# Kernel tuning notes

Hardware: AMD Instinct MI355X
Metric: run time of the kernel (lower is better)

The kernel has to match this reference:

```python
import jax, jax.numpy as jnp
import numpy as np

B, L, P, C, K, NL, DF = 32, 512, 96, 512, 8, 2, 512
CK = C // K
EPS = 1e-5


def setup_inputs() -> dict:
    key = jax.random.key(0)
    ks = jax.random.split(key, 6)
    s = lambda k, shape, fan: jax.random.normal(k, shape, jnp.float32) / np.float32(np.sqrt(fan))
    return dict(
        x=jax.random.normal(ks[0], (B, L, C), jnp.float32),
        cluster_ids=jnp.arange(C, dtype=jnp.int32),
        rev_w=jnp.ones((C,), jnp.float32),
        rev_b=jnp.zeros((C,), jnp.float32),
        Wt=s(ks[1], (K, NL, L, L), L),
        bt=jnp.zeros((K, NL, L), jnp.float32),
        ln1_g=jnp.ones((K, NL, CK), jnp.float32),
        ln1_b=jnp.zeros((K, NL, CK), jnp.float32),
        Wf1=s(ks[2], (K, NL, CK, DF), CK),
        bf1=jnp.zeros((K, NL, DF), jnp.float32),
        Wf2=s(ks[3], (K, NL, DF, CK), DF),
        bf2=jnp.zeros((K, NL, CK), jnp.float32),
        ln2_g=jnp.ones((K, NL, CK), jnp.float32),
        ln2_b=jnp.zeros((K, NL, CK), jnp.float32),
        Wout=s(ks[4], (K, L, P), L),
        bout=jnp.zeros((K, P), jnp.float32),
    )


def _ln(y, g, b):
    # y: [K,B,L,Ck]; g,b: [K,Ck] -- per-cluster layernorm over channel dim
    m = y.mean(-1, keepdims=True)
    v = y.var(-1, keepdims=True)
    return (y - m) * jax.lax.rsqrt(v + EPS) * g[:, None, None, :] + b[:, None, None, :]


def reference(x, cluster_ids, rev_w, rev_b, Wt, bt, ln1_g, ln1_b,
              Wf1, bf1, Wf2, bf2, ln2_g, ln2_b, Wout, bout):
    # RevIN norm (instance norm over time axis)
    mean = x.mean(axis=1, keepdims=True)
    std = jnp.sqrt(x.var(axis=1, keepdims=True) + EPS)
    xn = (x - mean) / std * rev_w + rev_b

    Kc = Wt.shape[0]
    Ck = cluster_ids.shape[0] // Kc
    assign = cluster_ids % Kc                 # hard cluster assignment per channel
    perm = jnp.argsort(assign)                # stable -> groups channels by cluster
    idx = perm.reshape(Kc, Ck)                # [K, Ck] channel ids per cluster

    # gather: [B,L,K,Ck] -> [K,B,L,Ck]
    xg = jnp.transpose(xn[:, :, idx], (2, 0, 1, 3))

    for l in range(Wt.shape[1]):
        # time mixing: Linear over seq dim, per cluster
        y = _ln(xg, ln1_g[:, l], ln1_b[:, l])
        y = jax.nn.relu(jnp.einsum('kblc,klm->kbmc', y, Wt[:, l]) + bt[:, l][:, None, :, None])
        xg = xg + y
        # feature mixing: Linear over channel dim, per cluster
        y = _ln(xg, ln2_g[:, l], ln2_b[:, l])
        y = jax.nn.relu(jnp.einsum('kblc,kcf->kblf', y, Wf1[:, l]) + bf1[:, l][:, None, None, :])
        y = jnp.einsum('kblf,kfc->kblc', y, Wf2[:, l]) + bf2[:, l][:, None, None, :]
        xg = xg + y

    # temporal projection seq_len -> pred_len: [K,B,P,Ck]
    out = jnp.einsum('kblc,klp->kbpc', xg, Wout) + bout[:, None, :, None]

    # scatter back to full channel layout
    flat = jnp.transpose(out, (1, 2, 0, 3)).reshape(x.shape[0], Wout.shape[-1], -1)
    full = jnp.zeros_like(flat).at[:, :, perm].set(flat)

    # RevIN denorm
    return (full - rev_b) / rev_w * std + mean
```

## Files before the change

kernel.cpp:

```cpp
#include <hip/hip_runtime.h>

typedef unsigned short u16;
typedef unsigned int   u32;
typedef __attribute__((ext_vector_type(8))) __bf16 bf16x8;
typedef __attribute__((ext_vector_type(4))) float  f32x4;

#define DEV __device__ __forceinline__

namespace {

constexpr int B_  = 32;
constexpr int L_  = 512;
constexpr int P_  = 96;
constexpr int C_  = 512;
constexpr int K_  = 8;
constexpr int NL_ = 2;
constexpr int DF_ = 512;
constexpr int CK_ = 64;
constexpr float EPS_ = 1e-5f;

DEV float bf2f(u16 u){ union { u32 i; float f; } t; t.i = ((u32)u) << 16; return t.f; }
DEV u16 f2bf(float f){ union { float f; u32 i; } t; t.f = f;
  u32 r = t.i + 0x7fffu + ((t.i >> 16) & 1u); return (u16)(r >> 16); }
DEV u16 f2bfn(float f){ __bf16 h = (__bf16)f; u16 u; __builtin_memcpy(&u, &h, 2); return u; }
DEV float LD(const void* p, size_t i, int bf){
  return bf ? bf2f(((const u16*)p)[i]) : ((const float*)p)[i];
}

__global__ __launch_bounds__(256) void k_probe(const u32* __restrict__ x, int* __restrict__ flag){
  int cnt = 0;
  for (int i = threadIdx.x; i < 4096; i += 256){
    u32 w = x[i];
    u32 e = (w >> 7) & 0xFFu;
    cnt += (e >= 0x70u && e <= 0x8Fu) ? 1 : 0;
  }
#pragma unroll
  for (int o = 32; o > 0; o >>= 1) cnt += __shfl_xor(cnt, o);
  __shared__ int s[4];
  if ((threadIdx.x & 63) == 0) s[threadIdx.x >> 6] = cnt;
  __syncthreads();
  if (threadIdx.x == 0) flag[0] = (s[0] + s[1] + s[2] + s[3] > 2048) ? 1 : 0;
}

__global__ __launch_bounds__(512) void k_sort(const int* __restrict__ cid, int* __restrict__ idx){
  __shared__ int bkt[C_];
  __shared__ int cnt[K_];
  __shared__ int off[K_];
  int c = threadIdx.x;
  int v = cid[c] % K_; if (v < 0) v += K_;
  bkt[c] = v;
  __syncthreads();
  if (c < K_){ int n = 0; for (int i = 0; i < C_; i++) n += (bkt[i] == c); cnt[c] = n; }
  __syncthreads();
  if (c == 0){ int s = 0; for (int k = 0; k < K_; k++){ off[k] = s; s += cnt[k]; } }
  __syncthreads();
  int r = 0;
  for (int i = 0; i < c; i++) r += (bkt[i] == bkt[c]);
  idx[off[bkt[c]] + r] = c;
}

__global__ __launch_bounds__(256) void k_trans(const void* __restrict__ in, u16* __restrict__ out,
                                               int R, int Cn, const int* __restrict__ flagp){
  __shared__ u16 t[32][36];
  int bf = *flagp;
  int z = blockIdx.z;
  int r0 = blockIdx.y * 32, c0 = blockIdx.x * 32;
  size_t base = (size_t)z * R * Cn;
  int tid = threadIdx.x;
  int i = tid >> 3, j4 = (tid & 7) * 4;
  size_t off = base + (size_t)(r0 + i) * Cn + c0 + j4;
  if (bf){
    ushort4 v = *reinterpret_cast<const ushort4*>((const u16*)in + off);
    t[i][j4 + 0] = v.x; t[i][j4 + 1] = v.y; t[i][j4 + 2] = v.z; t[i][j4 + 3] = v.w;
  } else {
    float4 v = *reinterpret_cast<const float4*>((const float*)in + off);
    t[i][j4 + 0] = f2bf(v.x); t[i][j4 + 1] = f2bf(v.y); t[i][j4 + 2] = f2bf(v.z); t[i][j4 + 3] = f2bf(v.w);
  }
  __syncthreads();
  ushort4 w;
  w.x = t[j4 + 0][i]; w.y = t[j4 + 1][i]; w.z = t[j4 + 2][i]; w.w = t[j4 + 3][i];
  *reinterpret_cast<ushort4*>(out + base + (size_t)(c0 + i) * R + r0 + j4) = w;
}

__global__ __launch_bounds__(512) void k_stats1(const void* __restrict__ x,
                                                float* __restrict__ psum, float* __restrict__ psq,
                                                const int* __restrict__ flagp){
  int bf = *flagp;
  int ls = blockIdx.x, b = blockIdx.y, c = threadIdx.x;
  size_t base = ((size_t)b * L_ + (size_t)ls * 32) * C_ + c;
  float s = 0.f, sq = 0.f;
#pragma unroll 8
  for (int l = 0; l < 32; l++){
    float v = LD(x, base + (size_t)l * C_, bf);
    s += v; sq += v * v;
  }
  int o = (b * 16 + ls) * C_ + c;
  psum[o] = s; psq[o] = sq;
}

__global__ __launch_bounds__(512) void k_stats2(const float* __restrict__ psum, const float* __restrict__ psq,
                                                const void* __restrict__ revw, const void* __restrict__ revb,
                                                float* __restrict__ meanw, float* __restrict__ stdw,
                                                float* __restrict__ scalew, float* __restrict__ biasw,
                                                const int* __restrict__ flagp){
  int bf = *flagp;
  int b = blockIdx.x, c = threadIdx.x;
  float s = 0.f, sq = 0.f;
#pragma unroll
  for (int i = 0; i < 16; i++){
    s  += psum[(b * 16 + i) * C_ + c];
    sq += psq [(b * 16 + i) * C_ + c];
  }
  float m = s * (1.f / L_);
  float var = sq * (1.f / L_) - m * m;
  float sd = sqrtf(var + EPS_);
  meanw[b * C_ + c] = m;
  stdw [b * C_ + c] = sd;
  float sc = LD(revw, c, bf) / sd;
  scalew[b * C_ + c] = sc;
  biasw [b * C_ + c] = LD(revb, c, bf) - m * sc;
}

__global__ __launch_bounds__(256) void k_gather(const void* __restrict__ x, const int* __restrict__ idx,
                                                const float* __restrict__ scalew, const float* __restrict__ biasw,
                                                float* __restrict__ xg, const int* __restrict__ flagp){
  __shared__ float row[576];
  int bf = *flagp;
  int lt = blockIdx.x, b = blockIdx.y;
  int tid = threadIdx.x;
  int oc0 = tid, oc1 = tid + 256;
  int c0 = idx[oc0], c1 = idx[oc1];
  float sc0 = scalew[b * C_ + c0], bs0 = biasw[b * C_ + c0];
  float sc1 = scalew[b * C_ + c1], bs1 = biasw[b * C_ + c1];
  int p0 = c0 + (c0 >> 3), p1 = c1 + (c1 >> 3);
  int k0 = oc0 >> 6, j0 = oc0 & 63;
  int k1 = oc1 >> 6, j1 = oc1 & 63;

  for (int r = 0; r < 16; r++){
    int l = lt * 16 + r;
    size_t base = ((size_t)b * L_ + l) * C_;
    if (bf){
      int i4 = tid * 2;
      ushort2 v = *reinterpret_cast<const ushort2*>((const u16*)x + base + i4);
      int a0 = i4, a1 = i4 + 1;
      row[a0 + (a0 >> 3)] = bf2f(v.x);
      row[a1 + (a1 >> 3)] = bf2f(v.y);
    } else {
      int i2 = tid * 2;
      float2 v = *reinterpret_cast<const float2*>((const float*)x + base + i2);
      int a0 = i2, a1 = i2 + 1;
      row[a0 + (a0 >> 3)] = v.x;
      row[a1 + (a1 >> 3)] = v.y;
    }
    __syncthreads();
    float o0 = row[p0] * sc0 + bs0;
    float o1 = row[p1] * sc1 + bs1;
    xg[(((size_t)k0 * B_ + b) * L_ + l) * CK_ + j0] = o0;
    xg[(((size_t)k1 * B_ + b) * L_ + l) * CK_ + j1] = o1;
    __syncthreads();
  }
}

__global__ __launch_bounds__(256) void k_lnt(const float* __restrict__ src, u16* __restrict__ dst,
                                             const void* __restrict__ g, const void* __restrict__ bb,
                                             int layer, int use_ln, const int* __restrict__ flagp){
  __shared__ float tile[64][65];
  int bf = *flagp;
  int z = blockIdx.x;
  int kb = z >> 3, lt = z & 7;
  int k = kb >> 5;
  const float* s = src + (size_t)kb * L_ * CK_ + (size_t)lt * 64 * CK_;
  int tid = threadIdx.x, lane = tid & 63, w = tid >> 6;
  float gj = 1.f, bj = 0.f;
  if (use_ln){
    gj = LD(g,  (size_t)(k * NL_ + layer) * CK_ + lane, bf);
    bj = LD(bb, (size_t)(k * NL_ + layer) * CK_ + lane, bf);
  }
  for (int i = 0; i < 16; i++){
    int row = w * 16 + i;
    float v = s[(size_t)row * CK_ + lane];
    float sum = v, sq = v * v;
#pragma unroll
    for (int o = 32; o > 0; o >>= 1){ sum += __shfl_xor(sum, o); sq += __shfl_xor(sq, o); }
    float nv = v;
    if (use_ln){
      float m = sum * (1.f / 64.f);
      float var = sq * (1.f / 64.f) - m * m;
      nv = (v - m) * rsqrtf(var + EPS_) * gj + bj;
    }
    tile[row][lane] = nv;
  }
  __syncthreads();
  int c = tid >> 2, seg = tid & 3;
  union { u16 s[8]; uint4 q; } u0, u1;
#pragma unroll
  for (int e = 0; e < 8; e++) u0.s[e] = f2bf(tile[seg * 16 + e][c]);
#pragma unroll
  for (int e = 0; e < 8; e++) u1.s[e] = f2bf(tile[seg * 16 + 8 + e][c]);
  u16* d = dst + (size_t)kb * CK_ * L_ + (size_t)c * L_ + lt * 64 + seg * 16;
  *reinterpret_cast<uint4*>(d)     = u0.q;
  *reinterpret_cast<uint4*>(d + 8) = u1.q;
}

__global__ __launch_bounds__(256, 4) void k_time(const u16* __restrict__ WtT, const u16* __restrict__ xpt,
                                                 float* __restrict__ xg, u16* __restrict__ xp,
                                                 const void* __restrict__ bt,
                                                 const void* __restrict__ ln2g, const void* __restrict__ ln2b,
                                                 int layer, const int* __restrict__ flagp){
  __shared__ u16 a_lds[128 * 40];
  __shared__ u16 b_lds[64 * 40];
  int bf = *flagp;
  int bid = blockIdx.x;
  int k = bid & 7, rr = bid >> 3;
  int b = rr & 31, mb = rr >> 5;
  int m0 = mb * 128;
  const int klb = k * NL_ + layer;
  const u16* A  = WtT + ((size_t)klb * L_ + m0) * L_;
  const u16* Bm = xpt + (size_t)(k * B_ + b) * CK_ * L_;
  int tid = threadIdx.x, lane = tid & 63, w = tid >> 6, grp = lane >> 4, ln = lane & 15;

  int sa0 = tid, sa1 = tid + 256;
  int ra0 = sa0 >> 2, qa0 = (sa0 & 3) * 8;
  int ra1 = sa1 >> 2, qa1 = (sa1 & 3) * 8;
  int rb0 = tid >> 2, qb0 = (tid & 3) * 8;

  f32x4 acc[2][4];
#pragma unroll
  for (int i = 0; i < 2; i++)
#pragma unroll
    for (int j = 0; j < 4; j++) acc[i][j] = (f32x4){0.f, 0.f, 0.f, 0.f};

  uint4 va0 = *reinterpret_cast<const uint4*>(A + (size_t)ra0 * L_ + qa0);
  uint4 va1 = *reinterpret_cast<const uint4*>(A + (size_t)ra1 * L_ + qa1);
  uint4 vb0 = *reinterpret_cast<const uint4*>(Bm + (size_t)rb0 * L_ + qb0);

  for (int kk = 0; kk < 16; kk++){
    *reinterpret_cast<uint4*>(&a_lds[ra0 * 40 + qa0]) = va0;
    *reinterpret_cast<uint4*>(&a_lds[ra1 * 40 + qa1]) = va1;
    *reinterpret_cast<uint4*>(&b_lds[rb0 * 40 + qb0]) = vb0;
    uint4 na0, na1, nb0;
    if (kk < 15){
      int c0 = (kk + 1) * 32;
      na0 = *reinterpret_cast<const uint4*>(A + (size_t)ra0 * L_ + c0 + qa0);
      na1 = *reinterpret_cast<const uint4*>(A + (size_t)ra1 * L_ + c0 + qa1);
      nb0 = *reinterpret_cast<const uint4*>(Bm + (size_t)rb0 * L_ + c0 + qb0);
    }
    __syncthreads();
    bf16x8 af[2], bfr[4];
#pragma unroll
    for (int mt = 0; mt < 2; mt++)
      af[mt] = *reinterpret_cast<bf16x8*>(&a_lds[(w * 32 + mt * 16 + ln) * 40 + grp * 8]);
#pragma unroll
    for (int ct = 0; ct < 4; ct++)
      bfr[ct] = *reinterpret_cast<bf16x8*>(&b_lds[(ct * 16 + ln) * 40 + grp * 8]);
#pragma unroll
    for (int mt = 0; mt < 2; mt++)
#pragma unroll
      for (int ct = 0; ct < 4; ct++)
        acc[mt][ct] = __builtin_amdgcn_mfma_f32_16x16x32_bf16(af[mt], bfr[ct], acc[mt][ct], 0, 0, 0);
    __syncthreads();
    va0 = na0; va1 = na1; vb0 = nb0;
  }

  float g2[4], b2[4];
#pragma unroll
  for (int ct = 0; ct < 4; ct++){
    int cc = ct * 16 + ln;
    g2[ct] = LD(ln2g, (size_t)klb * CK_ + cc, bf);
    b2[ct] = LD(ln2b, (size_t)klb * CK_ + cc, bf);
  }
  float* xgp = xg + (size_t)(k * B_ + b) * L_ * CK_;
  u16*  xpw = xp + (size_t)(k * B_ + b) * L_ * CK_;
#pragma unroll
  for (int mt = 0; mt < 2; mt++){
#pragma unroll
    for (int r = 0; r < 4; r++){
      int m = m0 + w * 32 + mt * 16 + grp * 4 + r;
      float bias = LD(bt, (size_t)klb * L_ + m, bf);
      float xn[4];
      float s = 0.f, sq = 0.f;
#pragma unroll
      for (int ct = 0; ct < 4; ct++){
        int cc = ct * 16 + ln;
        float y = fmaxf(acc[mt][ct][r] + bias, 0.f);
        float v = xgp[(size_t)m * CK_ + cc] + y;
        xgp[(size_t)m * CK_ + cc] = v;
        xn[ct] = v; s += v; sq += v * v;
      }
#pragma unroll
      for (int o = 1; o < 16; o <<= 1){ s += __shfl_xor(s, o); sq += __shfl_xor(sq, o); }
      float mean = s * (1.f / 64.f);
      float var = sq * (1.f / 64.f) - mean * mean;
      float rstd = rsqrtf(var + EPS_);
#pragma unroll
      for (int ct = 0; ct < 4; ct++){
        int cc = ct * 16 + ln;
        xpw[(size_t)m * CK_ + cc] = f2bfn((xn[ct] - mean) * rstd * g2[ct] + b2[ct]);
      }
    }
  }
}

__global__ __launch_bounds__(512, 4) void k_feat(const u16* __restrict__ xp, const u16* __restrict__ w1t,
                                                 const u16* __restrict__ w2t, float* __restrict__ xg,
                                                 const void* __restrict__ bf1, const void* __restrict__ bf2,
                                                 const void* __restrict__ ln1g, const void* __restrict__ ln1b,
                                                 u16* __restrict__ xsout, int layer,
                                                 const int* __restrict__ flagp){
  __shared__ u16 sm[256 * 72];
  __shared__ u16 wl[2][64 * 72];
  int bf = *flagp;
  int lt = blockIdx.x, b = blockIdx.y, k = blockIdx.z;
  int kb = k * B_ + b;
  const u16* xpp = xp + ((size_t)kb * L_ + lt * 256) * CK_;
  const u16* w1p = w1t + (size_t)(k * NL_ + layer) * DF_ * CK_;
  const u16* w2p = w2t + (size_t)(k * NL_ + layer) * CK_ * DF_;
  int tid = threadIdx.x, lane = tid & 63, w = tid >> 6, grp = lane >> 4, ln = lane & 15;
  int wr0 = tid >> 3, wq0 = (tid & 7) * 8;

#pragma unroll
  for (int s = tid; s < 2048; s += 512){
    int row = s >> 3, q = s & 7;
    *reinterpret_cast<uint4*>(&sm[row * 72 + q * 8]) =
      *reinterpret_cast<const uint4*>(xpp + (size_t)row * CK_ + q * 8);
  }
  uint4 g1a = *reinterpret_cast<const uint4*>(w1p + (size_t)wr0 * CK_ + wq0);
  uint4 g2a = *reinterpret_cast<const uint4*>(w2p + (size_t)wr0 * DF_ + wq0);
  __syncthreads();
  bf16x8 af[2][2];
#pragma unroll
  for (int mt = 0; mt < 2; mt++)
#pragma unroll
    for (int ks = 0; ks < 2; ks++)
      af[mt][ks] = *reinterpret_cast<bf16x8*>(&sm[(w * 32 + mt * 16 + ln) * 72 + ks * 32 + grp * 8]);
  __syncthreads();

  f32x4 acc2[2][4];
#pragma unroll
  for (int i = 0; i < 2; i++)
#pragma unroll
    for (int j = 0; j < 4; j++) acc2[i][j] = (f32x4){0.f, 0.f, 0.f, 0.f};

  const int klb = (k * NL_ + layer);
#pragma unroll
  for (int ft = 0; ft < 8; ft++){
    *reinterpret_cast<uint4*>(&wl[0][wr0 * 72 + wq0]) = g1a;
    *reinterpret_cast<uint4*>(&wl[1][wr0 * 72 + wq0]) = g2a;
    if (ft < 7){
      g1a = *reinterpret_cast<const uint4*>(w1p + (size_t)((ft + 1) * 64 + wr0) * CK_ + wq0);
      g2a = *reinterpret_cast<const uint4*>(w2p + (size_t)wr0 * DF_ + (ft + 1) * 64 + wq0);
    }
    __syncthreads();

    f32x4 acc1[2][4];
#pragma unroll
    for (int i = 0; i < 2; i++)
#pragma unroll
      for (int j = 0; j < 4; j++) acc1[i][j] = (f32x4){0.f, 0.f, 0.f, 0.f};
#pragma unroll
    for (int ks = 0; ks < 2; ks++)
#pragma unroll
      for (int n = 0; n < 4; n++){
        bf16x8 bb = *reinterpret_cast<bf16x8*>(&wl[0][(n * 16 + ln) * 72 + ks * 32 + grp * 8]);
#pragma unroll
        for (int mt = 0; mt < 2; mt++)
          acc1[mt][n] = __builtin_amdgcn_mfma_f32_16x16x32_bf16(af[mt][ks], bb, acc1[mt][n], 0, 0, 0);
      }
#pragma unroll
    for (int n = 0; n < 4; n++){
      float bias = LD(bf1, (size_t)klb * DF_ + ft * 64 + n * 16 + ln, bf);
#pragma unroll
      for (int mt = 0; mt < 2; mt++)
#pragma unroll
        for (int r = 0; r < 4; r++){
          float v = fmaxf(acc1[mt][n][r] + bias, 0.f);
          sm[(w * 32 + mt * 16 + grp * 4 + r) * 72 + n * 16 + ln] = f2bfn(v);
        }
    }
#pragma unroll
    for (int ks = 0; ks < 2; ks++){
      bf16x8 hh[2];
#pragma unroll
      for (int mt = 0; mt < 2; mt++)
        hh[mt] = *reinterpret_cast<bf16x8*>(&sm[(w * 32 + mt * 16 + ln) * 72 + ks * 32 + grp * 8]);
#pragma unroll
      for (int n = 0; n < 4; n++){
        bf16x8 bb = *reinterpret_cast<bf16x8*>(&wl[1][(n * 16 + ln) * 72 + ks * 32 + grp * 8]);
#pragma unroll
        for (int mt = 0; mt < 2; mt++)
          acc2[mt][n] = __builtin_amdgcn_mfma_f32_16x16x32_bf16(hh[mt], bb, acc2[mt][n], 0, 0, 0);
      }
    }
    __syncthreads();
  }

  const int next = layer + 1;
  const int use_ln = (next < NL_);
  float g1v[4], b1v[4], b2v[4];
#pragma unroll
  for (int n = 0; n < 4; n++){
    int cc = n * 16 + ln;
    b2v[n] = LD(bf2, (size_t)klb * CK_ + cc, bf);
    if (use_ln){
      g1v[n] = LD(ln1g, (size_t)(k * NL_ + next) * CK_ + cc, bf);
      b1v[n] = LD(ln1b, (size_t)(k * NL_ + next) * CK_ + cc, bf);
    } else { g1v[n] = 1.f; b1v[n] = 0.f; }
  }
  float* xgp = xg + ((size_t)kb * L_ + lt * 256) * CK_;
#pragma unroll
  for (int mt = 0; mt < 2; mt++){
#pragma unroll
    for (int r = 0; r < 4; r++){
      int rl = w * 32 + mt * 16 + grp * 4 + r;
      float v[4];
      float s = 0.f, sq = 0.f;
#pragma unroll
      for (int n = 0; n < 4; n++){
        int cc = n * 16 + ln;
        float t = xgp[(size_t)rl * CK_ + cc] + acc2[mt][n][r] + b2v[n];
        if (use_ln) xgp[(size_t)rl * CK_ + cc] = t;
        v[n] = t; s += t; sq += t * t;
      }
      float mean = 0.f, rstd = 1.f;
      if (use_ln){
#pragma unroll
        for (int o = 1; o < 16; o <<= 1){ s += __shfl_xor(s, o); sq += __shfl_xor(sq, o); }
        mean = s * (1.f / 64.f);
        float var = sq * (1.f / 64.f) - mean * mean;
        rstd = rsqrtf(var + EPS_);
      }
#pragma unroll
      for (int n = 0; n < 4; n++){
        int cc = n * 16 + ln;
        sm[cc * 264 + rl] = f2bfn((v[n] - mean) * rstd * g1v[n] + b1v[n]);
      }
    }
  }
  __syncthreads();
  u16* xsw = xsout + (size_t)kb * CK_ * L_ + lt * 256;
#pragma unroll
  for (int i = 0; i < 4; i++){
    int s = tid + i * 512;
    int c = s >> 5, off = (s & 31) * 8;
    *reinterpret_cast<uint4*>(xsw + (size_t)c * L_ + off) =
      *reinterpret_cast<uint4*>(&sm[c * 264 + off]);
  }
}

__global__ __launch_bounds__(384) void k_out(const u16* __restrict__ WoT, const u16* __restrict__ xgt,
                                             const int* __restrict__ idx, const void* __restrict__ bout,
                                             const void* __restrict__ revw, const void* __restrict__ revb,
                                             const float* __restrict__ meanw, const float* __restrict__ stdw,
                                             void* __restrict__ out, const int* __restrict__ flagp){
  __shared__ u16 a_lds[96 * 40];
  __shared__ u16 b_lds[64 * 40];
  int bf = *flagp;
  int b = blockIdx.x, k = blockIdx.y;
  int kb = k * B_ + b;
  const u16* A  = WoT + (size_t)k * P_ * L_;
  const u16* Bm = xgt + (size_t)kb * CK_ * L_;
  int tid = threadIdx.x, lane = tid & 63, w = tid >> 6, grp = lane >> 4, ln = lane & 15;
  f32x4 acc[4];
#pragma unroll
  for (int j = 0; j < 4; j++) acc[j] = (f32x4){0.f, 0.f, 0.f, 0.f};

  for (int kk = 0; kk < 16; kk++){
    {
      int row = tid >> 2, q = tid & 3;
      *reinterpret_cast<uint4*>(&a_lds[row * 40 + q * 8]) =
        *reinterpret_cast<const uint4*>(A + (size_t)row * L_ + kk * 32 + q * 8);
    }
    if (tid < 256){
      int row = tid >> 2, q = tid & 3;
      *reinterpret_cast<uint4*>(&b_lds[row * 40 + q * 8]) =
        *reinterpret_cast<const uint4*>(Bm + (size_t)row * L_ + kk * 32 + q * 8);
    }
    __syncthreads();
    bf16x8 af = *reinterpret_cast<bf16x8*>(&a_lds[(w * 16 + ln) * 40 + grp * 8]);
#pragma unroll
    for (int n = 0; n < 4; n++){
      bf16x8 bfr = *reinterpret_cast<bf16x8*>(&b_lds[(n * 16 + ln) * 40 + grp * 8]);
      acc[n] = __builtin_amdgcn_mfma_f32_16x16x32_bf16(af, bfr, acc[n], 0, 0, 0);
    }
    __syncthreads();
  }
#pragma unroll
  for (int n = 0; n < 4; n++){
    int j = n * 16 + ln;
    int c = idx[k * CK_ + j];
    float rw = LD(revw, c, bf), rb = LD(revb, c, bf);
    float sd = stdw[b * C_ + c], mn = meanw[b * C_ + c];
#pragma unroll
    for (int r = 0; r < 4; r++){
      int p = w * 16 + grp * 4 + r;
      float y = acc[n][r] + LD(bout, (size_t)k * P_ + p, bf);
      float val = (y - rb) / rw * sd + mn;
      size_t oi = ((size_t)b * P_ + p) * C_ + c;
      if (bf) ((u16*)out)[oi] = f2bf(val);
      else    ((float*)out)[oi] = val;
    }
  }
}

}

extern "C" void kernel_launch(void* const* d_in, const int* in_sizes, int n_in,
                              void* d_out, int out_size, void* d_ws, size_t ws_size,
                              hipStream_t stream){
  const void* x    = d_in[0];
  const int*  cid  = (const int*)d_in[1];
  const void* revw = d_in[2];
  const void* revb = d_in[3];
  const void* Wt   = d_in[4];
  const void* bt   = d_in[5];
  const void* ln1g = d_in[6];
  const void* ln1b = d_in[7];
  const void* Wf1  = d_in[8];
  const void* bf1  = d_in[9];
  const void* Wf2  = d_in[10];
  const void* bf2  = d_in[11];
  const void* ln2g = d_in[12];
  const void* ln2b = d_in[13];
  const void* Wout = d_in[14];
  const void* bout = d_in[15];
  char* ws = (char*)d_ws;

  int*   flag   = (int*)  (ws + 0);
  int*   idxp   = (int*)  (ws + 64);
  float* meanw  = (float*)(ws + 4096);
  float* stdw   = (float*)(ws + 69632);
  float* scalew = (float*)(ws + 135168);
  float* biasw  = (float*)(ws + 200704);
  float* psum   = (float*)(ws + 266240);
  float* psq    = (float*)(ws + 1314816);
  float* xg     = (float*)(ws + 2363392);
  u16*   xs     = (u16*)  (ws + 35917824);
  u16*   WtT    = (u16*)  (ws + 52695040);
  u16*   Wf1T   = (u16*)  (ws + 61083648);
  u16*   Wf2T   = (u16*)  (ws + 62132224);
  u16*   WoT    = (u16*)  (ws + 63180800);
  u16*   xp2    = (u16*)  (ws + 63967232);

  k_probe<<<1, 256, 0, stream>>>((const u32*)x, flag);
  k_sort<<<1, 512, 0, stream>>>(cid, idxp);
  k_trans<<<dim3(16, 16, 16), 256, 0, stream>>>(Wt,   WtT,  512, 512, flag);
  k_trans<<<dim3(16,  2, 16), 256, 0, stream>>>(Wf1,  Wf1T,  64, 512, flag);
  k_trans<<<dim3( 2, 16, 16), 256, 0, stream>>>(Wf2,  Wf2T, 512,  64, flag);
  k_trans<<<dim3( 3, 16,  8), 256, 0, stream>>>(Wout, WoT,  512,  96, flag);
  k_stats1<<<dim3(16, 32), 512, 0, stream>>>(x, psum, psq, flag);
  k_stats2<<<32, 512, 0, stream>>>(psum, psq, revw, revb, meanw, stdw, scalew, biasw, flag);
  k_gather<<<dim3(32, 32), 256, 0, stream>>>(x, idxp, scalew, biasw, xg, flag);

  k_lnt<<<2048, 256, 0, stream>>>(xg, xs, ln1g, ln1b, 0, 1, flag);
  for (int layer = 0; layer < NL_; layer++){
    k_time<<<1024, 256, 0, stream>>>(WtT, xs, xg, xp2, bt, ln2g, ln2b, layer, flag);
    k_feat<<<dim3(2, 32, 8), 512, 0, stream>>>(xp2, Wf1T, Wf2T, xg, bf1, bf2,
                                               ln1g, ln1b, xs, layer, flag);
  }

  k_out<<<dim3(32, 8), 384, 0, stream>>>(WoT, xs, idxp, bout, revw, revb, meanw, stdw, d_out, flag);
}
```

Measured before the change: 239.7 us.

## Fuse time-mixing and feature-mixing kernels into one per-layer kernel

Merges k_time and k_feat into a single k_mix kernel. Each block computes the time-mixing GEMM for a 128-row tile, keeps the LN2-normalized tile in shared memory and runs the feature MLP on it directly. This removes the bf16 intermediate round trip through global memory and one launch per layer. It ping-pongs the transposed activation buffers between the two layer launches. In exchange, feature mixing now runs in 256-thread blocks with more shared memory reuse and larger per-block weight loading, which may reduce occupancy.

```diff
diff --git a/kernel.cpp b/kernel.cpp
--- a/kernel.cpp
+++ b/kernel.cpp
@@ -202,21 +202,31 @@
   *reinterpret_cast<uint4*>(d + 8) = u1.q;
 }
 
-__global__ __launch_bounds__(256, 4) void k_time(const u16* __restrict__ WtT, const u16* __restrict__ xpt,
-                                                 float* __restrict__ xg, u16* __restrict__ xp,
-                                                 const void* __restrict__ bt,
-                                                 const void* __restrict__ ln2g, const void* __restrict__ ln2b,
-                                                 int layer, const int* __restrict__ flagp){
-  __shared__ u16 a_lds[128 * 40];
-  __shared__ u16 b_lds[64 * 40];
+__global__ __launch_bounds__(256, 4) void k_mix(const u16* __restrict__ WtT, const u16* __restrict__ xin,
+                                                float* __restrict__ xg,
+                                                const void* __restrict__ bt,
+                                                const void* __restrict__ ln2g, const void* __restrict__ ln2b,
+                                                const u16* __restrict__ w1t, const u16* __restrict__ w2t,
+                                                const void* __restrict__ bf1, const void* __restrict__ bf2,
+                                                const void* __restrict__ ln1g, const void* __restrict__ ln1b,
+                                                u16* __restrict__ xout, int layer,
+                                                const int* __restrict__ flagp){
+  __shared__ __align__(16) char lds[36864];
+  u16* a_lds = (u16*)lds;
+  u16* b_lds = (u16*)(lds + 10240);
+  u16* sm    = (u16*)lds;
+  u16* wl    = (u16*)(lds + 18432);
   int bf = *flagp;
   int bid = blockIdx.x;
   int k = bid & 7, rr = bid >> 3;
   int b = rr & 31, mb = rr >> 5;
   int m0 = mb * 128;
   const int klb = k * NL_ + layer;
+  int kb = k * B_ + b;
   const u16* A  = WtT + ((size_t)klb * L_ + m0) * L_;
-  const u16* Bm = xpt + (size_t)(k * B_ + b) * CK_ * L_;
+  const u16* Bm = xin + (size_t)kb * CK_ * L_;
+  const u16* w1p = w1t + (size_t)klb * DF_ * CK_;
+  const u16* w2p = w2t + (size_t)klb * CK_ * DF_;
   int tid = threadIdx.x, lane = tid & 63, w = tid >> 6, grp = lane >> 4, ln = lane & 15;
 
   int sa0 = tid, sa1 = tid + 256;
@@ -262,77 +272,60 @@
     va0 = na0; va1 = na1; vb0 = nb0;
   }
 
-  float g2[4], b2[4];
-#pragma unroll
-  for (int ct = 0; ct < 4; ct++){
-    int cc = ct * 16 + ln;
-    g2[ct] = LD(ln2g, (size_t)klb * CK_ + cc, bf);
-    b2[ct] = LD(ln2b, (size_t)klb * CK_ + cc, bf);
-  }
-  float* xgp = xg + (size_t)(k * B_ + b) * L_ * CK_;
-  u16*  xpw = xp + (size_t)(k * B_ + b) * L_ * CK_;
-#pragma unroll
-  for (int mt = 0; mt < 2; mt++){
-#pragma unroll
-    for (int r = 0; r < 4; r++){
-      int m = m0 + w * 32 + mt * 16 + grp * 4 + r;
-      float bias = LD(bt, (size_t)klb * L_ + m, bf);
-      float xn[4];
-      float s = 0.f, sq = 0.f;
-#pragma unroll
-      for (int ct = 0; ct < 4; ct++){
-        int cc = ct * 16 + ln;
-        float y = fmaxf(acc[mt][ct][r] + bias, 0.f);
-        float v = xgp[(size_t)m * CK_ + cc] + y;
-        xgp[(size_t)m * CK_ + cc] = v;
-        xn[ct] = v; s += v; sq += v * v;
+  int wr0 = tid >> 3, wq0 = (tid & 7) * 8;
+  int wr1 = wr0 + 32;
+  uint4 g1a = *reinterpret_cast<const uint4*>(w1p + (size_t)wr0 * CK_ + wq0);
+  uint4 g1b = *reinterpret_cast<const uint4*>(w1p + (size_t)wr1 * CK_ + wq0);
+  uint4 g2a = *reinterpret_cast<const uint4*>(w2p + (size_t)wr0 * DF_ + wq0);
+  uint4 g2b = *reinterpret_cast<const uint4*>(w2p + (size_t)wr1 * DF_ + wq0);
+
+  {
+    float g2[4], b2[4];
+#pragma unroll
+    for (int ct = 0; ct < 4; ct++){
+      int cc = ct * 16 + ln;
+      g2[ct] = LD(ln2g, (size_t)klb * CK_ + cc, bf);
+      b2[ct] = LD(ln2b, (size_t)klb * CK_ + cc, bf);
+    }
+    float* xgp = xg + (size_t)kb * L_ * CK_;
+#pragma unroll
+    for (int mt = 0; mt < 2; mt++){
+#pragma unroll
+      for (int r = 0; r < 4; r++){
+        int rl = w * 32 + mt * 16 + grp * 4 + r;
+        int m = m0 + rl;
+        float bias = LD(bt, (size_t)klb * L_ + m, bf);
+        float xn[4];
+        float s = 0.f, sq = 0.f;
+#pragma unroll
+        for (int ct = 0; ct < 4; ct++){
+          int cc = ct * 16 + ln;
+          float y = fmaxf(acc[mt][ct][r] + bias, 0.f);
+          float v = xgp[(size_t)m * CK_ + cc] + y;
+          xgp[(size_t)m * CK_ + cc] = v;
+          xn[ct] = v; s += v; sq += v * v;
+        }
+#pragma unroll
+        for (int o = 1; o < 16; o <<= 1){ s += __shfl_xor(s, o); sq += __shfl_xor(sq, o); }
+        float mean = s * (1.f / 64.f);
+        float var = sq * (1.f / 64.f) - mean * mean;
+        float rstd = rsqrtf(var + EPS_);
+#pragma unroll
+        for (int ct = 0; ct < 4; ct++){
+          int cc = ct * 16 + ln;
+          sm[rl * 72 + cc] = f2bfn((xn[ct] - mean) * rstd * g2[ct] + b2[ct]);
+        }
       }
-#pragma unroll
-      for (int o = 1; o < 16; o <<= 1){ s += __shfl_xor(s, o); sq += __shfl_xor(sq, o); }
-      float mean = s * (1.f / 64.f);
-      float var = sq * (1.f / 64.f) - mean * mean;
-      float rstd = rsqrtf(var + EPS_);
-#pragma unroll
-      for (int ct = 0; ct < 4; ct++){
-        int cc = ct * 16 + ln;
-        xpw[(size_t)m * CK_ + cc] = f2bfn((xn[ct] - mean) * rstd * g2[ct] + b2[ct]);
-      }
-    }
-  }
-}
-
-__global__ __launch_bounds__(512, 4) void k_feat(const u16* __restrict__ xp, const u16* __restrict__ w1t,
-                                                 const u16* __restrict__ w2t, float* __restrict__ xg,
-                                                 const void* __restrict__ bf1, const void* __restrict__ bf2,
-                                                 const void* __restrict__ ln1g, const void* __restrict__ ln1b,
-                                                 u16* __restrict__ xsout, int layer,
-                                                 const int* __restrict__ flagp){
-  __shared__ u16 sm[256 * 72];
-  __shared__ u16 wl[2][64 * 72];
-  int bf = *flagp;
-  int lt = blockIdx.x, b = blockIdx.y, k = blockIdx.z;
-  int kb = k * B_ + b;
-  const u16* xpp = xp + ((size_t)kb * L_ + lt * 256) * CK_;
-  const u16* w1p = w1t + (size_t)(k * NL_ + layer) * DF_ * CK_;
-  const u16* w2p = w2t + (size_t)(k * NL_ + layer) * CK_ * DF_;
-  int tid = threadIdx.x, lane = tid & 63, w = tid >> 6, grp = lane >> 4, ln = lane & 15;
-  int wr0 = tid >> 3, wq0 = (tid & 7) * 8;
-
-#pragma unroll
-  for (int s = tid; s < 2048; s += 512){
-    int row = s >> 3, q = s & 7;
-    *reinterpret_cast<uint4*>(&sm[row * 72 + q * 8]) =
-      *reinterpret_cast<const uint4*>(xpp + (size_t)row * CK_ + q * 8);
-  }
-  uint4 g1a = *reinterpret_cast<const uint4*>(w1p + (size_t)wr0 * CK_ + wq0);
-  uint4 g2a = *reinterpret_cast<const uint4*>(w2p + (size_t)wr0 * DF_ + wq0);
-  __syncthreads();
-  bf16x8 af[2][2];
+    }
+  }
+  __syncthreads();
+
+  bf16x8 faf[2][2];
 #pragma unroll
   for (int mt = 0; mt < 2; mt++)
 #pragma unroll
     for (int ks = 0; ks < 2; ks++)
-      af[mt][ks] = *reinterpret_cast<bf16x8*>(&sm[(w * 32 + mt * 16 + ln) * 72 + ks * 32 + grp * 8]);
+      faf[mt][ks] = *reinterpret_cast<bf16x8*>(&sm[(w * 32 + mt * 16 + ln) * 72 + ks * 32 + grp * 8]);
   __syncthreads();
 
   f32x4 acc2[2][4];
@@ -341,14 +334,17 @@
 #pragma unroll
     for (int j = 0; j < 4; j++) acc2[i][j] = (f32x4){0.f, 0.f, 0.f, 0.f};
 
-  const int klb = (k * NL_ + layer);
 #pragma unroll
   for (int ft = 0; ft < 8; ft++){
-    *reinterpret_cast<uint4*>(&wl[0][wr0 * 72 + wq0]) = g1a;
-    *reinterpret_cast<uint4*>(&wl[1][wr0 * 72 + wq0]) = g2a;
+    *reinterpret_cast<uint4*>(&wl[wr0 * 72 + wq0]) = g1a;
+    *reinterpret_cast<uint4*>(&wl[wr1 * 72 + wq0]) = g1b;
+    *reinterpret_cast<uint4*>(&wl[4608 + wr0 * 72 + wq0]) = g2a;
+    *reinterpret_cast<uint4*>(&wl[4608 + wr1 * 72 + wq0]) = g2b;
     if (ft < 7){
       g1a = *reinterpret_cast<const uint4*>(w1p + (size_t)((ft + 1) * 64 + wr0) * CK_ + wq0);
+      g1b = *reinterpret_cast<const uint4*>(w1p + (size_t)((ft + 1) * 64 + wr1) * CK_ + wq0);
       g2a = *reinterpret_cast<const uint4*>(w2p + (size_t)wr0 * DF_ + (ft + 1) * 64 + wq0);
+      g2b = *reinterpret_cast<const uint4*>(w2p + (size_t)wr1 * DF_ + (ft + 1) * 64 + wq0);
     }
     __syncthreads();
 
@@ -361,10 +357,10 @@
     for (int ks = 0; ks < 2; ks++)
 #pragma unroll
       for (int n = 0; n < 4; n++){
-        bf16x8 bb = *reinterpret_cast<bf16x8*>(&wl[0][(n * 16 + ln) * 72 + ks * 32 + grp * 8]);
+        bf16x8 bb = *reinterpret_cast<bf16x8*>(&wl[(n * 16 + ln) * 72 + ks * 32 + grp * 8]);
 #pragma unroll
         for (int mt = 0; mt < 2; mt++)
-          acc1[mt][n] = __builtin_amdgcn_mfma_f32_16x16x32_bf16(af[mt][ks], bb, acc1[mt][n], 0, 0, 0);
+          acc1[mt][n] = __builtin_amdgcn_mfma_f32_16x16x32_bf16(faf[mt][ks], bb, acc1[mt][n], 0, 0, 0);
       }
 #pragma unroll
     for (int n = 0; n < 4; n++){
@@ -385,7 +381,7 @@
         hh[mt] = *reinterpret_cast<bf16x8*>(&sm[(w * 32 + mt * 16 + ln) * 72 + ks * 32 + grp * 8]);
 #pragma unroll
       for (int n = 0; n < 4; n++){
-        bf16x8 bb = *reinterpret_cast<bf16x8*>(&wl[1][(n * 16 + ln) * 72 + ks * 32 + grp * 8]);
+        bf16x8 bb = *reinterpret_cast<bf16x8*>(&wl[4608 + (n * 16 + ln) * 72 + ks * 32 + grp * 8]);
 #pragma unroll
         for (int mt = 0; mt < 2; mt++)
           acc2[mt][n] = __builtin_amdgcn_mfma_f32_16x16x32_bf16(hh[mt], bb, acc2[mt][n], 0, 0, 0);
@@ -406,7 +402,7 @@
       b1v[n] = LD(ln1b, (size_t)(k * NL_ + next) * CK_ + cc, bf);
     } else { g1v[n] = 1.f; b1v[n] = 0.f; }
   }
-  float* xgp = xg + ((size_t)kb * L_ + lt * 256) * CK_;
+  float* xgp = xg + ((size_t)kb * L_ + m0) * CK_;
 #pragma unroll
   for (int mt = 0; mt < 2; mt++){
 #pragma unroll
@@ -432,18 +428,18 @@
 #pragma unroll
       for (int n = 0; n < 4; n++){
         int cc = n * 16 + ln;
-        sm[cc * 264 + rl] = f2bfn((v[n] - mean) * rstd * g1v[n] + b1v[n]);
+        sm[cc * 136 + rl] = f2bfn((v[n] - mean) * rstd * g1v[n] + b1v[n]);
       }
     }
   }
   __syncthreads();
-  u16* xsw = xsout + (size_t)kb * CK_ * L_ + lt * 256;
+  u16* xsw = xout + (size_t)kb * CK_ * L_ + m0;
 #pragma unroll
   for (int i = 0; i < 4; i++){
-    int s = tid + i * 512;
-    int c = s >> 5, off = (s & 31) * 8;
+    int s = tid + i * 256;
+    int c = s >> 4, off = (s & 15) * 8;
     *reinterpret_cast<uint4*>(xsw + (size_t)c * L_ + off) =
-      *reinterpret_cast<uint4*>(&sm[c * 264 + off]);
+      *reinterpret_cast<uint4*>(&sm[c * 136 + off]);
   }
 }
 
@@ -534,12 +530,12 @@
   float* psum   = (float*)(ws + 266240);
   float* psq    = (float*)(ws + 1314816);
   float* xg     = (float*)(ws + 2363392);
-  u16*   xs     = (u16*)  (ws + 35917824);
+  u16*   xsA    = (u16*)  (ws + 35917824);
   u16*   WtT    = (u16*)  (ws + 52695040);
   u16*   Wf1T   = (u16*)  (ws + 61083648);
   u16*   Wf2T   = (u16*)  (ws + 62132224);
   u16*   WoT    = (u16*)  (ws + 63180800);
-  u16*   xp2    = (u16*)  (ws + 63967232);
+  u16*   xsB    = (u16*)  (ws + 63967232);
 
   k_probe<<<1, 256, 0, stream>>>((const u32*)x, flag);
   k_sort<<<1, 512, 0, stream>>>(cid, idxp);
@@ -551,12 +547,11 @@
   k_stats2<<<32, 512, 0, stream>>>(psum, psq, revw, revb, meanw, stdw, scalew, biasw, flag);
   k_gather<<<dim3(32, 32), 256, 0, stream>>>(x, idxp, scalew, biasw, xg, flag);
 
-  k_lnt<<<2048, 256, 0, stream>>>(xg, xs, ln1g, ln1b, 0, 1, flag);
-  for (int layer = 0; layer < NL_; layer++){
-    k_time<<<1024, 256, 0, stream>>>(WtT, xs, xg, xp2, bt, ln2g, ln2b, layer, flag);
-    k_feat<<<dim3(2, 32, 8), 512, 0, stream>>>(xp2, Wf1T, Wf2T, xg, bf1, bf2,
-                                               ln1g, ln1b, xs, layer, flag);
-  }
-
-  k_out<<<dim3(32, 8), 384, 0, stream>>>(WoT, xs, idxp, bout, revw, revb, meanw, stdw, d_out, flag);
-}
+  k_lnt<<<2048, 256, 0, stream>>>(xg, xsA, ln1g, ln1b, 0, 1, flag);
+  k_mix<<<1024, 256, 0, stream>>>(WtT, xsA, xg, bt, ln2g, ln2b, Wf1T, Wf2T,
+                                  bf1, bf2, ln1g, ln1b, xsB, 0, flag);
+  k_mix<<<1024, 256, 0, stream>>>(WtT, xsB, xg, bt, ln2g, ln2b, Wf1T, Wf2T,
+                                  bf1, bf2, ln1g, ln1b, xsA, 1, flag);
+
+  k_out<<<dim3(32, 8), 384, 0, stream>>>(WoT, xsA, idxp, bout, revw, revb, meanw, stdw, d_out, flag);
+}
```

New measurement: 224.7 us. 1.07x faster.
